# Kernel tuning notes

Measured on AMD Instinct MI355X. Metric: run time of the kernel, lower is better.

The kernel has to match this reference:

```python
import jax, jax.numpy as jnp
import numpy as np

P = 10      # qubits
LQ = 4      # re-uploading layers
B = 4096    # batch
HID = 32    # readout hidden
DIM = 2 ** P


def _rz(t):
    t = jnp.asarray(t, jnp.float32)
    e = jnp.exp(-0.5j * t.astype(jnp.complex64))
    z = jnp.zeros_like(e)
    return jnp.stack([jnp.stack([e, z], -1), jnp.stack([z, jnp.conj(e)], -1)], -2)


def _rx(t):
    t = jnp.asarray(t, jnp.float32)
    c = jnp.cos(0.5 * t).astype(jnp.complex64)
    s = jnp.sin(0.5 * t).astype(jnp.complex64)
    return jnp.stack([jnp.stack([c, -1j * s], -1), jnp.stack([-1j * s, c], -1)], -2)


def _ry(t):
    t = jnp.asarray(t, jnp.float32)
    c = jnp.cos(0.5 * t).astype(jnp.complex64)
    s = jnp.sin(0.5 * t).astype(jnp.complex64)
    return jnp.stack([jnp.stack([c, -s], -1), jnp.stack([s, c], -1)], -2)


def _apply_1q(state, U, k):
    # state [B, 2^P] complex, U [B,2,2]; wire 0 = most-significant bit (PennyLane order)
    b = state.shape[0]
    s = state.reshape(b, 2 ** k, 2, -1)
    s = jnp.einsum('bij,bajc->baic', U, s)
    return s.reshape(b, -1)


def _apply_cnot(state, c, t):
    b = state.shape[0]
    a, d = min(c, t), max(c, t)
    s = state.reshape(b, 2 ** a, 2, 2 ** (d - a - 1), 2, -1)
    if c == a:  # control = smaller wire index (axis 2), target at axis 4
        hi = jnp.flip(s[:, :, 1], axis=3)  # [b,pre,mid,2,post] -> flip target bit
        s = jnp.stack([s[:, :, 0], hi], axis=2)
    else:       # control = larger wire index (axis 4), target at axis 2
        hi = jnp.flip(s[:, :, :, :, 1], axis=2)  # [b,pre,2,mid,post] -> flip target bit
        s = jnp.stack([s[:, :, :, :, 0], hi], axis=4)
    return s.reshape(b, -1)


def _meas_signs(p):
    # rows 0..p-1: Z_k signs; rows p..2p-1: Z_k Z_{(k+1)%p} signs
    idx = np.arange(2 ** p)
    bits = (idx[None, :] >> (p - 1 - np.arange(p)[:, None])) & 1
    z = (1.0 - 2.0 * bits).astype(np.float32)            # [p, 2^p]
    zz = z * np.roll(z, -1, axis=0)                      # [p, 2^p]
    return jnp.asarray(np.concatenate([z, zz], axis=0))  # [2p, 2^p]


MEAS = _meas_signs(P)


def _circuit_feats(theta, rot_weights, enc_scale, enc_bias):
    b = theta.shape[0]
    # Hadamard on every wire of |0...0> -> uniform superposition
    state = jnp.full((b, DIM), 1.0 / np.sqrt(DIM), dtype=jnp.complex64)
    for l in range(LQ):
        for k in range(P):
            t0 = enc_scale[l, k, 0] * theta[:, k] + enc_bias[l, k, 0]
            t1 = enc_scale[l, k, 1] * theta[:, k] + enc_bias[l, k, 1]
            U_enc = jnp.einsum('bij,bjk->bik', _rx(t1), _rz(t0))  # RX(t1) RZ(t0)
            w = rot_weights[l, k]
            # PennyLane Rot(phi,theta,omega) = RZ(omega) RY(theta) RZ(phi)
            U_rot = _rz(w[2]) @ _ry(w[1]) @ _rz(w[0])
            U = jnp.einsum('ij,bjk->bik', U_rot, U_enc)
            state = _apply_1q(state, U, k)
        for k in range(P):
            state = _apply_cnot(state, k, (k + 1) % P)
    probs = jnp.abs(state) ** 2              # [B, 2^P]
    return probs @ MEAS.T                    # [B, 2P] expectation values


def setup_inputs() -> dict:
    key = jax.random.key(0)
    ks = jax.random.split(key, 4)
    theta = jax.random.uniform(ks[0], (B, P), jnp.float32, -np.pi, np.pi)
    rot_weights = 0.02 * jax.random.normal(ks[1], (LQ, P, 3), dtype=jnp.float32)
    enc_scale = jnp.ones((LQ, P, 2), jnp.float32)   # clamp(0.5,1.5) of ones = ones
    enc_bias = jnp.zeros((LQ, P, 2), jnp.float32)
    n_meas = 2 * P
    W1 = jax.random.normal(ks[2], (HID, n_meas), dtype=jnp.float32) / np.sqrt(n_meas)
    b1 = jnp.zeros((HID,), jnp.float32)
    W2 = jax.random.normal(ks[3], (1, HID), dtype=jnp.float32) / np.sqrt(HID)
    b2 = jnp.zeros((1,), jnp.float32)
    return dict(theta=theta, rot_weights=rot_weights, enc_scale=enc_scale,
                enc_bias=enc_bias, W1=W1, b1=b1, W2=W2, b2=b2)


def reference(theta, rot_weights, enc_scale, enc_bias, W1, b1, W2, b2):
    feats = _circuit_feats(theta, rot_weights, enc_scale, enc_bias)
    h = jax.nn.silu(feats @ W1.T + b1)
    return (h @ W2.T + b2)[:, 0]  # [B]
```

## Files before the change

kernel.cpp:

```cpp
#include <hip/hip_runtime.h>
#include <math.h>

#define NQ   10
#define NLAY 4
#define BATCH 4096
#define HID  32
#define NM   20

typedef float    f2  __attribute__((ext_vector_type(2)));
typedef unsigned u2v __attribute__((ext_vector_type(2)));

struct Tables {
    unsigned col[NLAY + 1][NQ];
    unsigned row[NLAY + 1][NQ];
};

constexpr Tables make_tables() {
    Tables t{};
    unsigned col[NQ] = {}, row[NQ] = {};
    for (int k = 0; k < NQ; ++k) { col[k] = 1u << (NQ - 1 - k); row[k] = 1u << (NQ - 1 - k); }
    for (int l = 0; l <= NLAY; ++l) {
        for (int k = 0; k < NQ; ++k) { t.col[l][k] = col[k]; t.row[l][k] = row[k]; }
        for (int k = 0; k < NQ; ++k) {
            int c = k, tg = (k + 1) % NQ;
            col[c] ^= col[tg];
            row[tg] ^= row[c];
        }
    }
    return t;
}

static constexpr Tables TB = make_tables();

struct cpx { float x, y; };
__device__ __forceinline__ cpx cxmul(cpx a, cpx b) {
    return { fmaf(a.x, b.x, -a.y * b.y), fmaf(a.x, b.y, a.y * b.x) };
}

__device__ __forceinline__ f2 mk2(float a, float b) { f2 r; r[0] = a; r[1] = b; return r; }
__device__ __forceinline__ f2 ffma(f2 a, f2 b, f2 c) { return __builtin_elementwise_fma(a, b, c); }

__device__ __forceinline__ f2 cmac(f2 acc, f2 a, f2 b) {
    acc = ffma(mk2(a[0], a[0]), b, acc);
    acc = ffma(mk2(-a[1], a[1]), mk2(b[1], b[0]), acc);
    return acc;
}

template<int CTRL>
__device__ __forceinline__ float dppf(float x) {
    return __int_as_float(__builtin_amdgcn_update_dpp(
        0, __float_as_int(x), CTRL, 0xF, 0xF, true));
}

template<unsigned M>
__device__ __forceinline__ float dpplo(float x) {
    static_assert(M < 16u, "dpplo handles masks 0..15");
    if constexpr (M == 0u)       return x;
    else if constexpr (M == 1u)  return dppf<0xB1>(x);
    else if constexpr (M == 2u)  return dppf<0x4E>(x);
    else if constexpr (M == 3u)  return dppf<0x1B>(x);
    else if constexpr (M == 7u)  return dppf<0x141>(x);
    else if constexpr (M == 8u)  return dppf<0x128>(x);
    else if constexpr (M == 15u) return dppf<0x140>(x);
    else if constexpr (M == 4u)  return dppf<0x141>(dppf<0x1B>(x));
    else if constexpr (M == 5u)  return dppf<0x141>(dppf<0x4E>(x));
    else if constexpr (M == 6u)  return dppf<0x141>(dppf<0xB1>(x));
    else if constexpr (M == 9u)  return dppf<0x128>(dppf<0xB1>(x));
    else if constexpr (M == 10u) return dppf<0x128>(dppf<0x4E>(x));
    else if constexpr (M == 11u) return dppf<0x128>(dppf<0x1B>(x));
    else if constexpr (M == 12u) return dppf<0x140>(dppf<0x1B>(x));
    else if constexpr (M == 13u) return dppf<0x140>(dppf<0x4E>(x));
    else                         return dppf<0x140>(dppf<0xB1>(x));
}

__device__ __forceinline__ float swap16sel(float x, bool sel16) {
#if __has_builtin(__builtin_amdgcn_permlane16_swap)
    u2v r = __builtin_amdgcn_permlane16_swap(__float_as_uint(x), __float_as_uint(x), false, false);
    return sel16 ? __uint_as_float(r[0]) : __uint_as_float(r[1]);
#else
    (void)sel16; return __shfl_xor(x, 16);
#endif
}
__device__ __forceinline__ float swap32sel(float x, bool sel32) {
#if __has_builtin(__builtin_amdgcn_permlane32_swap)
    u2v r = __builtin_amdgcn_permlane32_swap(__float_as_uint(x), __float_as_uint(x), false, false);
    return sel32 ? __uint_as_float(r[0]) : __uint_as_float(r[1]);
#else
    (void)sel32; return __shfl_xor(x, 32);
#endif
}
__device__ __forceinline__ float redfold16(float x) {
#if __has_builtin(__builtin_amdgcn_permlane16_swap)
    u2v r = __builtin_amdgcn_permlane16_swap(__float_as_uint(x), __float_as_uint(x), false, false);
    return __uint_as_float(r[0]) + __uint_as_float(r[1]);
#else
    return x + __shfl_xor(x, 16);
#endif
}
__device__ __forceinline__ float redfold32(float x) {
#if __has_builtin(__builtin_amdgcn_permlane32_swap)
    u2v r = __builtin_amdgcn_permlane32_swap(__float_as_uint(x), __float_as_uint(x), false, false);
    return __uint_as_float(r[0]) + __uint_as_float(r[1]);
#else
    return x + __shfl_xor(x, 32);
#endif
}

template<unsigned M>
__device__ __forceinline__ float xlane(float x, bool sel16, bool sel32) {
    if constexpr (M == 0u) return x;
    else if constexpr ((M & 48u) == 48u) return __shfl_xor(x, (int)M);
    else {
        float y = dpplo<M & 15u>(x);
        if constexpr ((M & 48u) == 16u)      y = swap16sel(y, sel16);
        else if constexpr ((M & 48u) == 32u) y = swap32sel(y, sel32);
        return y;
    }
}

template<int L, int K>
__device__ __forceinline__ void apply_gate(f2 (&st)[16],
                                           const float4 (*gm)[2], const int lane,
                                           const bool sel16, const bool sel32) {
    constexpr unsigned v  = TB.col[L][K];
    constexpr unsigned m  = TB.row[L][K];
    constexpr unsigned vl = v >> 4;
    constexpr int      vr = (int)(v & 15u);
    constexpr unsigned ml = m >> 4;
    constexpr int      mr = (int)(m & 15u);
    constexpr int      gi = L * NQ + K;

    int laneP = 0;
    if constexpr (ml != 0) laneP = __popc((unsigned)lane & ml) & 1;
    const float4 A = gm[gi][laneP];
    const f2 ocA = mk2(A.x, A.y), pcA = mk2(A.z, A.w);
    f2 ocB = ocA, pcB = pcA;
    if constexpr (mr != 0) {
        const float4 B = gm[gi][laneP ^ 1];
        ocB = mk2(B.x, B.y); pcB = mk2(B.z, B.w);
    }

    f2 pv[16];
    #pragma unroll
    for (int r = 0; r < 16; ++r) {
        const f2 q = st[r ^ vr];
        if constexpr (vl == 0u) pv[r] = q;
        else pv[r] = mk2(xlane<vl>(q[0], sel16, sel32), xlane<vl>(q[1], sel16, sel32));
    }
    #pragma unroll
    for (int r = 0; r < 16; ++r) {
        const int pr = __builtin_popcount((unsigned)(r & mr)) & 1;
        const f2 oc = pr ? ocB : ocA;
        const f2 pc = pr ? pcB : pcA;
        f2 acc = mk2(0.f, 0.f);
        acc = cmac(acc, oc, st[r]);
        acc = cmac(acc, pc, pv[r]);
        st[r] = acc;
    }
}

__global__ __launch_bounds__(256, 4) void qrh_kernel(
    const float* __restrict__ theta, const float* __restrict__ rotw,
    const float* __restrict__ escale, const float* __restrict__ ebias,
    const float* __restrict__ W1, const float* __restrict__ b1,
    const float* __restrict__ W2, const float* __restrict__ b2,
    float* __restrict__ out)
{
    __shared__ float4 gmat[4][NLAY * NQ][2];
    __shared__ float4 wtab[4][NQ];

    const int tid  = threadIdx.x;
    const int lane = tid & 63;
    const int wv   = tid >> 6;
    const int b    = blockIdx.x * 4 + wv;

    bool sel16 = false, sel32 = false;
#if __has_builtin(__builtin_amdgcn_permlane16_swap)
    {
        u2v r = __builtin_amdgcn_permlane16_swap((unsigned)lane, (unsigned)lane, false, false);
        sel16 = (((lane & 16) != 0) == (r[0] == (unsigned)(lane & ~16)));
    }
#endif
#if __has_builtin(__builtin_amdgcn_permlane32_swap)
    {
        u2v r = __builtin_amdgcn_permlane32_swap((unsigned)lane, (unsigned)lane, false, false);
        sel32 = (((lane & 32) != 0) == (r[0] == (unsigned)(lane & ~32)));
    }
#endif

    if (lane < NLAY * NQ) {
        const int g = lane, l = g / NQ, k = g % NQ;
        const float th = theta[b * NQ + k];
        const int e2 = (l * NQ + k) * 2;
        const float t0 = escale[e2 + 0] * th + ebias[e2 + 0];
        const float t1 = escale[e2 + 1] * th + ebias[e2 + 1];
        float sn0, c0, sn1, c1;
        __sincosf(0.5f * t0, &sn0, &c0);
        __sincosf(0.5f * t1, &sn1, &c1);
        const f2 E00 = mk2( c1 * c0,  -c1 * sn0);
        const f2 E01 = mk2( sn1 * sn0, -sn1 * c0);
        const f2 E10 = mk2(-sn1 * sn0, -sn1 * c0);
        const f2 E11 = mk2( c1 * c0,   c1 * sn0);
        const int r3 = (l * NQ + k) * 3;
        const float w0 = rotw[r3 + 0], w1 = rotw[r3 + 1], w2 = rotw[r3 + 2];
        float cw, sw, ca0, sa0, ca1, sa1;
        __sincosf(0.5f * w1, &sw, &cw);
        __sincosf(0.5f * (w0 + w2), &sa0, &ca0);
        __sincosf(0.5f * (w0 - w2), &sa1, &ca1);
        const f2 R00 = mk2( cw * ca0, -cw * sa0);
        const f2 R01 = mk2(-sw * ca1, -sw * sa1);
        const f2 R10 = mk2( sw * ca1, -sw * sa1);
        const f2 R11 = mk2( cw * ca0,  cw * sa0);
        auto cm = [](f2 a, f2 bb) { return mk2(a[0]*bb[0] - a[1]*bb[1], a[0]*bb[1] + a[1]*bb[0]); };
        const f2 U00 = cm(R00, E00) + cm(R01, E10);
        const f2 U01 = cm(R00, E01) + cm(R01, E11);
        const f2 U10 = cm(R10, E00) + cm(R11, E10);
        const f2 U11 = cm(R10, E01) + cm(R11, E11);
        gmat[wv][g][0] = make_float4(U00[0], U00[1], U01[0], U01[1]);
        gmat[wv][g][1] = make_float4(U11[0], U11[1], U10[0], U10[1]);
        if (l == 0) {
            const float inv = 0.70710678118654752f;
            const f2 al = (U00 + U01) * inv;
            const f2 be = (U10 + U11) * inv;
            wtab[wv][k] = make_float4(al[0], al[1], be[0], be[1]);
        }
    }
    __syncthreads();

    f2 st[16];
    {
        cpx pre;
        {
            const float4 q = wtab[wv][0];
            pre = ((lane >> 5) & 1) ? cpx{q.z, q.w} : cpx{q.x, q.y};
            #pragma unroll
            for (int k = 1; k < 6; ++k) {
                const float4 t = wtab[wv][k];
                const cpx w_ = ((lane >> (5 - k)) & 1) ? cpx{t.z, t.w} : cpx{t.x, t.y};
                pre = cxmul(pre, w_);
            }
        }
        const float4 q6 = wtab[wv][6], q7 = wtab[wv][7];
        const float4 q8 = wtab[wv][8], q9 = wtab[wv][9];
        const cpx w6[2] = {{q6.x, q6.y}, {q6.z, q6.w}};
        const cpx w7[2] = {{q7.x, q7.y}, {q7.z, q7.w}};
        const cpx w8[2] = {{q8.x, q8.y}, {q8.z, q8.w}};
        const cpx w9[2] = {{q9.x, q9.y}, {q9.z, q9.w}};
        cpx ph[4], tlo[4];
        #pragma unroll
        for (int a = 0; a < 4; ++a) {
            ph[a]  = cxmul(pre, cxmul(w6[a >> 1], w7[a & 1]));
            tlo[a] = cxmul(w8[a >> 1], w9[a & 1]);
        }
        #pragma unroll
        for (int r = 0; r < 16; ++r) {
            const cpx a0 = cxmul(ph[r >> 2], tlo[r & 3]);
            st[r] = mk2(a0.x, a0.y);
        }
    }

    const float4 (*gm)[2] = gmat[wv];

    #define GATE(L,K) apply_gate<L,K>(st, gm, lane, sel16, sel32);
    #define LAYER(L) GATE(L,0) GATE(L,1) GATE(L,2) GATE(L,3) GATE(L,4) \
                     GATE(L,5) GATE(L,6) GATE(L,7) GATE(L,8) GATE(L,9)
    LAYER(1)
    LAYER(2)
    LAYER(3)
    #undef LAYER
    #undef GATE

    float w[16];
    #pragma unroll
    for (int r = 0; r < 16; ++r) {
        const f2 sq = st[r] * st[r];
        w[r] = sq[0] + sq[1];
    }
    #pragma unroll
    for (int bit = 1; bit < 16; bit <<= 1) {
        #pragma unroll
        for (int j = 0; j < 16; ++j) {
            if (!(j & bit)) {
                const float a = w[j], c = w[j | bit];
                w[j] = a + c; w[j | bit] = a - c;
            }
        }
    }

    float feats[NM];
    #pragma unroll
    for (int f = 0; f < NM; ++f) {
        const unsigned M = (f < NQ) ? TB.row[NLAY][f]
                                    : (TB.row[NLAY][f - NQ] ^ TB.row[NLAY][(f - NQ + 1) % NQ]);
        const int Ml = (int)(M >> 4), Mj = (int)(M & 15u);
        const float s = w[Mj];
        const int lsgn = __popc((unsigned)lane & (unsigned)Ml) & 1;
        feats[f] = lsgn ? -s : s;
    }
    #pragma unroll
    for (int f = 0; f < NM; ++f) {
        float v = feats[f];
        v += dppf<0xB1>(v);
        v += dppf<0x4E>(v);
        v += dppf<0x141>(v);
        v += dppf<0x128>(v);
        v = redfold16(v);
        v = redfold32(v);
        feats[f] = v;
    }

    float part = 0.f;
    if (lane < HID) {
        float acc = b1[lane];
        #pragma unroll
        for (int mm = 0; mm < NM; ++mm) acc = fmaf(feats[mm], W1[lane * NM + mm], acc);
        const float sg = 1.f / (1.f + __expf(-acc));
        part = acc * sg * W2[lane];
    }
    part += dppf<0xB1>(part);
    part += dppf<0x4E>(part);
    part += dppf<0x141>(part);
    part += dppf<0x128>(part);
    part = redfold16(part);
    part = redfold32(part);
    if (lane == 0) out[b] = part + b2[0];
}

extern "C" void kernel_launch(void* const* d_in, const int* in_sizes, int n_in,
                              void* d_out, int out_size, void* d_ws, size_t ws_size,
                              hipStream_t stream) {
    (void)in_sizes; (void)n_in; (void)out_size; (void)d_ws; (void)ws_size;
    const float* theta = (const float*)d_in[0];
    const float* rotw  = (const float*)d_in[1];
    const float* esc   = (const float*)d_in[2];
    const float* ebi   = (const float*)d_in[3];
    const float* W1    = (const float*)d_in[4];
    const float* b1    = (const float*)d_in[5];
    const float* W2    = (const float*)d_in[6];
    const float* b2    = (const float*)d_in[7];
    float* out = (float*)d_out;

    qrh_kernel<<<BATCH / 4, 256, 0, stream>>>(theta, rotw, esc, ebi, W1, b1, W2, b2, out);
}
```

Before: 100.2 us.

## Split each sample's statevector across two waves with LDS exchange

Each batch element now runs on two wavefronts, each holding 8 amplitudes per lane instead of 16, so registers per thread halve and occupancy can rise (waves_per_eu 7). Gates acting on the wave-selecting bit exchange amplitudes through shared memory with block barriers, and the final features are combined across waves via LDS before the readout MLP. Launch changes to one 128-thread block per sample. The trade-off is extra barriers and LDS traffic for gates touching the lowest bit, plus a second wave sitting idle during readout.

```diff
diff --git a/kernel.cpp b/kernel.cpp
--- a/kernel.cpp
+++ b/kernel.cpp
@@ -108,30 +108,31 @@
 
 template<unsigned M>
 __device__ __forceinline__ float xlane(float x, bool sel16, bool sel32) {
-    if constexpr (M == 0u) return x;
-    else if constexpr ((M & 48u) == 48u) return __shfl_xor(x, (int)M);
-    else {
-        float y = dpplo<M & 15u>(x);
-        if constexpr ((M & 48u) == 16u)      y = swap16sel(y, sel16);
-        else if constexpr ((M & 48u) == 32u) y = swap32sel(y, sel32);
-        return y;
-    }
-}
+    float y = dpplo<M & 15u>(x);
+    if constexpr ((M & 16u) != 0u) y = swap16sel(y, sel16);
+    if constexpr ((M & 32u) != 0u) y = swap32sel(y, sel32);
+    return y;
+}
+
+#define XSTRIDE 18
 
 template<int L, int K>
-__device__ __forceinline__ void apply_gate(f2 (&st)[16],
-                                           const float4 (*gm)[2], const int lane,
+__device__ __forceinline__ void apply_gate(f2 (&st)[8], const float4 (*gm)[2],
+                                           float* xbuf, const int lane, const int wv,
                                            const bool sel16, const bool sel32) {
-    constexpr unsigned v  = TB.col[L][K];
-    constexpr unsigned m  = TB.row[L][K];
-    constexpr unsigned vl = v >> 4;
-    constexpr int      vr = (int)(v & 15u);
-    constexpr unsigned ml = m >> 4;
-    constexpr int      mr = (int)(m & 15u);
-    constexpr int      gi = L * NQ + K;
+    constexpr unsigned v     = TB.col[L][K];
+    constexpr unsigned m     = TB.row[L][K];
+    constexpr unsigned vlane = (v >> 4) & 63u;
+    constexpr int      vr    = (int)((v >> 1) & 7u);
+    constexpr int      vw    = (int)(v & 1u);
+    constexpr unsigned mlane = (m >> 4) & 63u;
+    constexpr int      mr    = (int)((m >> 1) & 7u);
+    constexpr int      mw    = (int)(m & 1u);
+    constexpr int      gi    = L * NQ + K;
 
     int laneP = 0;
-    if constexpr (ml != 0) laneP = __popc((unsigned)lane & ml) & 1;
+    if constexpr (mlane != 0u || mw != 0)
+        laneP = (__popc((unsigned)lane & mlane) ^ (wv & mw)) & 1;
     const float4 A = gm[gi][laneP];
     const f2 ocA = mk2(A.x, A.y), pcA = mk2(A.z, A.w);
     f2 ocB = ocA, pcB = pcA;
@@ -140,15 +141,30 @@
         ocB = mk2(B.x, B.y); pcB = mk2(B.z, B.w);
     }
 
-    f2 pv[16];
-    #pragma unroll
-    for (int r = 0; r < 16; ++r) {
-        const f2 q = st[r ^ vr];
-        if constexpr (vl == 0u) pv[r] = q;
-        else pv[r] = mk2(xlane<vl>(q[0], sel16, sel32), xlane<vl>(q[1], sel16, sel32));
-    }
-    #pragma unroll
-    for (int r = 0; r < 16; ++r) {
+    f2 pv[8];
+    if constexpr (vw != 0) {
+        float* slot = xbuf + (unsigned)(wv * 64 + lane) * XSTRIDE;
+        #pragma unroll
+        for (int r = 0; r < 8; ++r) *(f2*)(slot + 2 * r) = st[r];
+        __syncthreads();
+        const float* ps = xbuf + (unsigned)((wv ^ 1) * 64 + (lane ^ (int)vlane)) * XSTRIDE;
+        #pragma unroll
+        for (int r = 0; r < 8; ++r) pv[r] = *(const f2*)(ps + 2 * (r ^ vr));
+        __syncthreads();
+    } else if constexpr (vlane != 0u) {
+        #pragma unroll
+        for (int r = 0; r < 8; ++r) {
+            const f2 q = st[r ^ vr];
+            pv[r] = mk2(xlane<vlane>(q[0], sel16, sel32),
+                        xlane<vlane>(q[1], sel16, sel32));
+        }
+    } else {
+        #pragma unroll
+        for (int r = 0; r < 8; ++r) pv[r] = st[r ^ vr];
+    }
+
+    #pragma unroll
+    for (int r = 0; r < 8; ++r) {
         const int pr = __builtin_popcount((unsigned)(r & mr)) & 1;
         const f2 oc = pr ? ocB : ocA;
         const f2 pc = pr ? pcB : pcA;
@@ -159,37 +175,41 @@
     }
 }
 
-__global__ __launch_bounds__(256, 4) void qrh_kernel(
+__global__ __launch_bounds__(128)
+__attribute__((amdgpu_waves_per_eu(7)))
+void qrh_kernel(
     const float* __restrict__ theta, const float* __restrict__ rotw,
     const float* __restrict__ escale, const float* __restrict__ ebias,
     const float* __restrict__ W1, const float* __restrict__ b1,
     const float* __restrict__ W2, const float* __restrict__ b2,
     float* __restrict__ out)
 {
-    __shared__ float4 gmat[4][NLAY * NQ][2];
-    __shared__ float4 wtab[4][NQ];
+    __shared__ float4 gmat[NLAY * NQ][2];
+    __shared__ float4 wtab[NQ];
+    __shared__ float  xbuf[2 * 64 * XSTRIDE];
+    __shared__ float  fbuf[NM];
 
     const int tid  = threadIdx.x;
     const int lane = tid & 63;
     const int wv   = tid >> 6;
-    const int b    = blockIdx.x * 4 + wv;
+    const int b    = blockIdx.x;
 
     bool sel16 = false, sel32 = false;
 #if __has_builtin(__builtin_amdgcn_permlane16_swap)
     {
         u2v r = __builtin_amdgcn_permlane16_swap((unsigned)lane, (unsigned)lane, false, false);
-        sel16 = (((lane & 16) != 0) == (r[0] == (unsigned)(lane & ~16)));
+        sel16 = (r[0] == (unsigned)(lane ^ 16));
     }
 #endif
 #if __has_builtin(__builtin_amdgcn_permlane32_swap)
     {
         u2v r = __builtin_amdgcn_permlane32_swap((unsigned)lane, (unsigned)lane, false, false);
-        sel32 = (((lane & 32) != 0) == (r[0] == (unsigned)(lane & ~32)));
-    }
-#endif
-
-    if (lane < NLAY * NQ) {
-        const int g = lane, l = g / NQ, k = g % NQ;
+        sel32 = (r[0] == (unsigned)(lane ^ 32));
+    }
+#endif
+
+    if (tid < NLAY * NQ) {
+        const int g = tid, l = g / NQ, k = g % NQ;
         const float th = theta[b * NQ + k];
         const int e2 = (l * NQ + k) * 2;
         const float t0 = escale[e2 + 0] * th + ebias[e2 + 0];
@@ -216,52 +236,50 @@
         const f2 U01 = cm(R00, E01) + cm(R01, E11);
         const f2 U10 = cm(R10, E00) + cm(R11, E10);
         const f2 U11 = cm(R10, E01) + cm(R11, E11);
-        gmat[wv][g][0] = make_float4(U00[0], U00[1], U01[0], U01[1]);
-        gmat[wv][g][1] = make_float4(U11[0], U11[1], U10[0], U10[1]);
+        gmat[g][0] = make_float4(U00[0], U00[1], U01[0], U01[1]);
+        gmat[g][1] = make_float4(U11[0], U11[1], U10[0], U10[1]);
         if (l == 0) {
             const float inv = 0.70710678118654752f;
             const f2 al = (U00 + U01) * inv;
             const f2 be = (U10 + U11) * inv;
-            wtab[wv][k] = make_float4(al[0], al[1], be[0], be[1]);
+            wtab[k] = make_float4(al[0], al[1], be[0], be[1]);
         }
     }
     __syncthreads();
 
-    f2 st[16];
+    f2 st[8];
     {
         cpx pre;
         {
-            const float4 q = wtab[wv][0];
+            const float4 q = wtab[0];
             pre = ((lane >> 5) & 1) ? cpx{q.z, q.w} : cpx{q.x, q.y};
             #pragma unroll
             for (int k = 1; k < 6; ++k) {
-                const float4 t = wtab[wv][k];
+                const float4 t = wtab[k];
                 const cpx w_ = ((lane >> (5 - k)) & 1) ? cpx{t.z, t.w} : cpx{t.x, t.y};
                 pre = cxmul(pre, w_);
             }
-        }
-        const float4 q6 = wtab[wv][6], q7 = wtab[wv][7];
-        const float4 q8 = wtab[wv][8], q9 = wtab[wv][9];
+            const float4 q9 = wtab[9];
+            const cpx w9v = wv ? cpx{q9.z, q9.w} : cpx{q9.x, q9.y};
+            pre = cxmul(pre, w9v);
+        }
+        const float4 q6 = wtab[6], q7 = wtab[7], q8 = wtab[8];
         const cpx w6[2] = {{q6.x, q6.y}, {q6.z, q6.w}};
         const cpx w7[2] = {{q7.x, q7.y}, {q7.z, q7.w}};
         const cpx w8[2] = {{q8.x, q8.y}, {q8.z, q8.w}};
-        const cpx w9[2] = {{q9.x, q9.y}, {q9.z, q9.w}};
-        cpx ph[4], tlo[4];
-        #pragma unroll
-        for (int a = 0; a < 4; ++a) {
-            ph[a]  = cxmul(pre, cxmul(w6[a >> 1], w7[a & 1]));
-            tlo[a] = cxmul(w8[a >> 1], w9[a & 1]);
-        }
-        #pragma unroll
-        for (int r = 0; r < 16; ++r) {
-            const cpx a0 = cxmul(ph[r >> 2], tlo[r & 3]);
-            st[r] = mk2(a0.x, a0.y);
-        }
-    }
-
-    const float4 (*gm)[2] = gmat[wv];
-
-    #define GATE(L,K) apply_gate<L,K>(st, gm, lane, sel16, sel32);
+        cpx ph[4];
+        #pragma unroll
+        for (int a = 0; a < 4; ++a) ph[a] = cxmul(cxmul(pre, w6[a >> 1]), w7[a & 1]);
+        #pragma unroll
+        for (int r = 0; r < 8; ++r) {
+            const cpx t = cxmul(ph[r >> 1], w8[r & 1]);
+            st[r] = mk2(t.x, t.y);
+        }
+    }
+
+    const float4 (*gm)[2] = gmat;
+
+    #define GATE(L,K) apply_gate<L,K>(st, gm, xbuf, lane, wv, sel16, sel32);
     #define LAYER(L) GATE(L,0) GATE(L,1) GATE(L,2) GATE(L,3) GATE(L,4) \
                      GATE(L,5) GATE(L,6) GATE(L,7) GATE(L,8) GATE(L,9)
     LAYER(1)
@@ -270,16 +288,16 @@
     #undef LAYER
     #undef GATE
 
-    float w[16];
-    #pragma unroll
-    for (int r = 0; r < 16; ++r) {
+    float w[8];
+    #pragma unroll
+    for (int r = 0; r < 8; ++r) {
         const f2 sq = st[r] * st[r];
         w[r] = sq[0] + sq[1];
     }
     #pragma unroll
-    for (int bit = 1; bit < 16; bit <<= 1) {
-        #pragma unroll
-        for (int j = 0; j < 16; ++j) {
+    for (int bit = 1; bit < 8; bit <<= 1) {
+        #pragma unroll
+        for (int j = 0; j < 8; ++j) {
             if (!(j & bit)) {
                 const float a = w[j], c = w[j | bit];
                 w[j] = a + c; w[j | bit] = a - c;
@@ -292,9 +310,11 @@
     for (int f = 0; f < NM; ++f) {
         const unsigned M = (f < NQ) ? TB.row[NLAY][f]
                                     : (TB.row[NLAY][f - NQ] ^ TB.row[NLAY][(f - NQ + 1) % NQ]);
-        const int Ml = (int)(M >> 4), Mj = (int)(M & 15u);
-        const float s = w[Mj];
-        const int lsgn = __popc((unsigned)lane & (unsigned)Ml) & 1;
+        const unsigned Mlane = (M >> 4) & 63u;
+        const int Mr = (int)((M >> 1) & 7u);
+        const int Mw = (int)(M & 1u);
+        const float s = w[Mr];
+        const int lsgn = (__popc((unsigned)lane & Mlane) ^ (wv & Mw)) & 1;
         feats[f] = lsgn ? -s : s;
     }
     #pragma unroll
@@ -309,21 +329,30 @@
         feats[f] = v;
     }
 
-    float part = 0.f;
-    if (lane < HID) {
-        float acc = b1[lane];
-        #pragma unroll
-        for (int mm = 0; mm < NM; ++mm) acc = fmaf(feats[mm], W1[lane * NM + mm], acc);
-        const float sg = 1.f / (1.f + __expf(-acc));
-        part = acc * sg * W2[lane];
-    }
-    part += dppf<0xB1>(part);
-    part += dppf<0x4E>(part);
-    part += dppf<0x141>(part);
-    part += dppf<0x128>(part);
-    part = redfold16(part);
-    part = redfold32(part);
-    if (lane == 0) out[b] = part + b2[0];
+    if (wv == 1 && lane == 0) {
+        #pragma unroll
+        for (int f = 0; f < NM; ++f) fbuf[f] = feats[f];
+    }
+    __syncthreads();
+    if (wv == 0) {
+        #pragma unroll
+        for (int f = 0; f < NM; ++f) feats[f] += fbuf[f];
+        float part = 0.f;
+        if (lane < HID) {
+            float acc = b1[lane];
+            #pragma unroll
+            for (int mm = 0; mm < NM; ++mm) acc = fmaf(feats[mm], W1[lane * NM + mm], acc);
+            const float sg = 1.f / (1.f + __expf(-acc));
+            part = acc * sg * W2[lane];
+        }
+        part += dppf<0xB1>(part);
+        part += dppf<0x4E>(part);
+        part += dppf<0x141>(part);
+        part += dppf<0x128>(part);
+        part = redfold16(part);
+        part = redfold32(part);
+        if (lane == 0) out[b] = part + b2[0];
+    }
 }
 
 extern "C" void kernel_launch(void* const* d_in, const int* in_sizes, int n_in,
@@ -340,5 +369,5 @@
     const float* b2    = (const float*)d_in[7];
     float* out = (float*)d_out;
 
-    qrh_kernel<<<BATCH / 4, 256, 0, stream>>>(theta, rotw, esc, ebi, W1, b1, W2, b2, out);
-}
+    qrh_kernel<<<BATCH, 128, 0, stream>>>(theta, rotw, esc, ebi, W1, b1, W2, b2, out);
+}
```

Measured after the change: 113.1 us. 12.9% more time.
